# Performance work log

Hardware: AMD Instinct MI355X
Metric: run time of the kernel (lower is better)

The kernel has to match this reference:

```python
import jax, jax.numpy as jnp
import numpy as np

NEG_SLOPE = 0.2  # PyG GATConv default leaky_relu slope


def _add_self_loops(edge_index, num_nodes):
    loop = jnp.arange(num_nodes, dtype=edge_index.dtype)
    return jnp.concatenate([edge_index, jnp.stack([loop, loop])], axis=1)


def _gat_conv(x, edge_index, W, a_src, a_dst, b, heads, out_c):
    # x: [N, Fin]; W: [Fin, heads*out_c]; a_src/a_dst: [heads, out_c]; b: [heads*out_c]
    N = x.shape[0]
    h = (x @ W).reshape(N, heads, out_c)                       # [N,H,C]
    src, dst = edge_index[0], edge_index[1]
    alpha_src = jnp.einsum('nhc,hc->nh', h, a_src)             # [N,H]
    alpha_dst = jnp.einsum('nhc,hc->nh', h, a_dst)             # [N,H]
    e = jax.nn.leaky_relu(alpha_src[src] + alpha_dst[dst], NEG_SLOPE)  # [E,H]
    # segment softmax over edges grouped by destination node
    m = jax.ops.segment_max(e, dst, num_segments=N)
    m = jnp.where(jnp.isfinite(m), m, jnp.zeros_like(m))
    ex = jnp.exp(e - m[dst])
    denom = jax.ops.segment_sum(ex, dst, num_segments=N)
    alpha = ex / (denom[dst] + 1e-16)                          # [E,H]
    out = jax.ops.segment_sum(h[src] * alpha[:, :, None], dst, num_segments=N)
    return out.reshape(N, heads * out_c) + b


def setup_inputs() -> dict:
    key = jax.random.key(0)
    ks = jax.random.split(key, 16)
    N, E, FIN, HID, HEADS, OUT = 50000, 800000, 128, 32, 4, 64
    x = jax.random.normal(ks[0], (N, FIN), dtype=jnp.float32)
    edge_index = jax.random.randint(ks[1], (2, E), 0, N, dtype=jnp.int64)
    s = 0.1
    inp = {
        'x': x, 'edge_index': edge_index,
        'W0': jax.random.normal(ks[2], (FIN, HEADS * HID), jnp.float32) * s,
        'asrc0': jax.random.normal(ks[3], (HEADS, HID), jnp.float32) * s,
        'adst0': jax.random.normal(ks[4], (HEADS, HID), jnp.float32) * s,
        'b0': jnp.zeros((HEADS * HID,), jnp.float32),
        'W1': jax.random.normal(ks[5], (HEADS * HID, HEADS * HID), jnp.float32) * s,
        'asrc1': jax.random.normal(ks[6], (HEADS, HID), jnp.float32) * s,
        'adst1': jax.random.normal(ks[7], (HEADS, HID), jnp.float32) * s,
        'b1': jnp.zeros((HEADS * HID,), jnp.float32),
        'W2': jax.random.normal(ks[8], (HEADS * HID, OUT), jnp.float32) * s,
        'asrc2': jax.random.normal(ks[9], (1, OUT), jnp.float32) * s,
        'adst2': jax.random.normal(ks[10], (1, OUT), jnp.float32) * s,
        'b2': jnp.zeros((OUT,), jnp.float32),
    }
    return inp


def reference(x, edge_index, W0, asrc0, adst0, b0, W1, asrc1, adst1, b1, W2, asrc2, adst2, b2):
    # Dropout is identity in eval mode.
    N = x.shape[0]
    ei = _add_self_loops(edge_index, N)
    h = _gat_conv(x, ei, W0, asrc0, adst0, b0, heads=4, out_c=32)
    h = jax.nn.relu(h)
    h = _gat_conv(h, ei, W1, asrc1, adst1, b1, heads=4, out_c=32)
    h = jax.nn.relu(h)
    out = _gat_conv(h, ei, W2, asrc2, adst2, b2, heads=1, out_c=64)
    return out
```

## Files before the change

kernel.cpp:

```cpp
#include <hip/hip_runtime.h>


#define NEG_SLOPE 0.2f

typedef _Float16 f16;
typedef f16 f16x8 __attribute__((ext_vector_type(8)));
typedef f16 f16x4 __attribute__((ext_vector_type(4)));
typedef f16 f16x2 __attribute__((ext_vector_type(2)));
typedef float f32x4 __attribute__((ext_vector_type(4)));

#define BSH 6
#define DLOWM 63
#define KEYBITS 22

__device__ __forceinline__ float lrelu(float v) { return v > 0.f ? v : NEG_SLOPE * v; }


__global__ void fill_zero_kernel(int* __restrict__ p, int n) {
    int i = blockIdx.x * blockDim.x + threadIdx.x;
    if (i < n) p[i] = 0;
}

__global__ __launch_bounds__(256) void bucket_count_kernel(const int* __restrict__ dst, int E,
                                                           int NBK, int* __restrict__ bcount) {
    __shared__ int lh[1024];
#pragma unroll
    for (int j = 0; j < 4; ++j) lh[threadIdx.x + j * 256] = 0;
    __syncthreads();
    int stride = gridDim.x * 256 * 4;
    for (int i = (blockIdx.x * 256 + threadIdx.x) * 4; i < E; i += stride) {
        int4 d = *(const int4*)&dst[i];
        atomicAdd(&lh[d.x >> BSH], 1);
        atomicAdd(&lh[d.y >> BSH], 1);
        atomicAdd(&lh[d.z >> BSH], 1);
        atomicAdd(&lh[d.w >> BSH], 1);
    }
    __syncthreads();
#pragma unroll
    for (int j = 0; j < 4; ++j) {
        int idx = threadIdx.x + j * 256;
        if (idx < NBK) {
            int v = lh[idx];
            if (v > 0) atomicAdd(&bcount[idx], v);
        }
    }
}

__global__ __launch_bounds__(256) void bucket_scan_kernel(const int* __restrict__ bcount, int NBK,
                                                          int* __restrict__ bbase,
                                                          int* __restrict__ bcursor,
                                                          int* __restrict__ offsets, int N) {
    int t = threadIdx.x;
    int chunk = (NBK + 255) / 256;
    int b0 = t * chunk, b1 = b0 + chunk;
    if (b0 > NBK) b0 = NBK;
    if (b1 > NBK) b1 = NBK;
    int s = 0;
    for (int i = b0; i < b1; ++i) s += bcount[i];
    int v = s;
    int lane = t & 63, wid = t >> 6;
#pragma unroll
    for (int off = 1; off < 64; off <<= 1) {
        int u = __shfl_up(v, off);
        if (lane >= off) v += u;
    }
    __shared__ int ws[4];
    if (lane == 63) ws[wid] = v;
    __syncthreads();
    int add = 0;
    for (int w = 0; w < wid; ++w) add += ws[w];
    v += add;
    int prefix = v - s;
    for (int i = b0; i < b1; ++i) {
        bbase[i] = prefix;
        bcursor[i] = prefix;
        prefix += bcount[i];
    }
    if (t == 255) {
        bbase[NBK] = v;
        offsets[N] = v;
    }
}

#define SC_TILE 4096
__global__ __launch_bounds__(256) void bucket_scatter_kernel(const int* __restrict__ src,
                                                             const int* __restrict__ dst, int E,
                                                             int* __restrict__ bcursor,
                                                             unsigned int* __restrict__ staging) {
    __shared__ int lh[1024];
    __shared__ int lcur[1024];
    int tid = threadIdx.x;
#pragma unroll
    for (int j = 0; j < 4; ++j) lh[tid + j * 256] = 0;
    __syncthreads();
    int base = blockIdx.x * SC_TILE + tid * 16;
    int sv[16], dv[16];
    bool act = base < E;
    if (act) {
#pragma unroll
        for (int q = 0; q < 4; ++q) {
            *(int4*)&sv[q * 4] = *(const int4*)&src[base + q * 4];
            *(int4*)&dv[q * 4] = *(const int4*)&dst[base + q * 4];
        }
#pragma unroll
        for (int j = 0; j < 16; ++j) atomicAdd(&lh[dv[j] >> BSH], 1);
    }
    __syncthreads();
#pragma unroll
    for (int j = 0; j < 4; ++j) {
        int idx = tid + j * 256;
        int c = lh[idx];
        if (c > 0) lcur[idx] = atomicAdd(&bcursor[idx], c);
    }
    __syncthreads();
    if (act) {
#pragma unroll
        for (int j = 0; j < 16; ++j) {
            int b = dv[j] >> BSH;
            int pos = atomicAdd(&lcur[b], 1);
            staging[pos] = (unsigned int)sv[j] | ((unsigned int)(dv[j] & DLOWM) << 16);
        }
    }
}

#define SORT_CAP 2048
#define MIDX(f) ((f) + ((f) >> 4))
__global__ __launch_bounds__(256) void bucket_sort_kernel(const unsigned int* __restrict__ staging,
                                                          const int* __restrict__ bbase,
                                                          int* __restrict__ offsets,
                                                          int* __restrict__ ssrc, int N) {
    __shared__ unsigned int bufA[SORT_CAP];
    __shared__ unsigned int bufB[SORT_CAP];
    __shared__ int mat[4096 + 256];
    __shared__ int lh[64];
    __shared__ int wsum[4];
    int b = blockIdx.x;
    int tid = threadIdx.x;
    int s = bbase[b], e = bbase[b + 1];
    int cnt = e - s;
    bool fits = cnt <= SORT_CAP;

    if (tid < 64) lh[tid] = 0;
    __syncthreads();
    if (fits) {
        for (int i = tid; i < cnt; i += 256) {
            unsigned int r = staging[s + i];
            bufA[i] = r;
            atomicAdd(&lh[r >> 16], 1);
        }
    } else {
        for (int i = tid; i < cnt; i += 256) atomicAdd(&lh[staging[s + i] >> 16], 1);
    }
    __syncthreads();

    int exc0 = 0;
    if (tid < 64) {
        int own = lh[tid];
        int v = own;
#pragma unroll
        for (int off = 1; off < 64; off <<= 1) {
            int u = __shfl_up(v, off);
            if (tid >= off) v += u;
        }
        exc0 = v - own;
        int dstn = (b << BSH) + tid;
        if (dstn < N) offsets[dstn] = s + exc0;
    }
    __syncthreads();

    int lane = tid & 63, wid = tid >> 6;
    if (fits) {
        unsigned int* in = bufA;
        unsigned int* out = bufB;
        int L = (cnt + 255) >> 8;
        int i0 = tid * L;
        int i1 = i0 + L;
        if (i0 > cnt) i0 = cnt;
        if (i1 > cnt) i1 = cnt;
        for (int sh = 0; sh < KEYBITS; sh += 4) {
            int c16[16];
#pragma unroll
            for (int d = 0; d < 16; ++d) c16[d] = 0;
            for (int i = i0; i < i1; ++i) c16[(in[i] >> sh) & 15]++;
#pragma unroll
            for (int d = 0; d < 16; ++d) mat[MIDX(d * 256 + tid)] = c16[d];
            __syncthreads();
            int base = tid * 16;
            int loc[16];
            int ssum = 0;
#pragma unroll
            for (int j = 0; j < 16; ++j) {
                loc[j] = ssum;
                ssum += mat[MIDX(base + j)];
            }
            int vv = ssum;
#pragma unroll
            for (int off = 1; off < 64; off <<= 1) {
                int u = __shfl_up(vv, off);
                if (lane >= off) vv += u;
            }
            if (lane == 63) wsum[wid] = vv;
            __syncthreads();
            int add2 = 0;
            for (int w = 0; w < wid; ++w) add2 += wsum[w];
            int exc2 = vv + add2 - ssum;
#pragma unroll
            for (int j = 0; j < 16; ++j) mat[MIDX(base + j)] = exc2 + loc[j];
            __syncthreads();
#pragma unroll
            for (int d = 0; d < 16; ++d) c16[d] = mat[MIDX(d * 256 + tid)];
            for (int i = i0; i < i1; ++i) {
                unsigned int r = in[i];
                int d = (r >> sh) & 15;
                out[c16[d]++] = r;
            }
            __syncthreads();
            unsigned int* tmp = in;
            in = out;
            out = tmp;
        }
        for (int i = tid; i < cnt; i += 256) {
            unsigned int r = bufA[i];
            int dlow = (r >> 16) & DLOWM;
            unsigned int full = (r & 0xFFFFu) | ((unsigned int)((b << BSH) | dlow) << 16);
            ssrc[s + i] = (int)full;
        }
    } else {
        if (tid < 64) lh[tid] = exc0;
        __syncthreads();
        for (int i = tid; i < cnt; i += 256) {
            unsigned int rec = staging[s + i];
            int dlow = rec >> 16;
            int r = atomicAdd(&lh[dlow], 1);
            unsigned int full = (rec & 0xFFFFu) | ((unsigned int)((b << BSH) | dlow) << 16);
            ssrc[s + r] = (int)full;
        }
    }
}


__global__ void split_w_kernel(const float* __restrict__ W0, const float* __restrict__ W1,
                               const float* __restrict__ W2, f16* __restrict__ w0h,
                               f16* __restrict__ w0l, f16* __restrict__ w1h,
                               f16* __restrict__ w1l, f16* __restrict__ w2h,
                               f16* __restrict__ w2l) {
    int idx = blockIdx.x * 256 + threadIdx.x;
    if (idx < 16384) {
        int k = idx >> 7, c = idx & 127;
        float v = W0[k * 128 + c];
        f16 h = (f16)v;
        w0h[c * 128 + k] = h;
        w0l[c * 128 + k] = (f16)(v - (float)h);
    } else if (idx < 32768) {
        int t = idx - 16384;
        int k = t >> 7, c = t & 127;
        float v = W1[k * 128 + c];
        f16 h = (f16)v;
        w1h[c * 128 + k] = h;
        w1l[c * 128 + k] = (f16)(v - (float)h);
    } else if (idx < 40960) {
        int t = idx - 32768;
        int k = t >> 6, c = t & 63;
        float v = W2[k * 64 + c];
        f16 h = (f16)v;
        w2h[c * 128 + k] = h;
        w2l[c * 128 + k] = (f16)(v - (float)h);
    }
}

template <int FOUT, int H_, bool F32A>
__global__ __launch_bounds__(256) void gemm_mfma_kernel(
    const f16* __restrict__ Ah, const f16* __restrict__ Al, const float* __restrict__ Af,
    const f16* __restrict__ Bh, const f16* __restrict__ Bl, const float* __restrict__ a_src,
    const float* __restrict__ a_dst, f16* __restrict__ H16, float* __restrict__ asrc,
    float* __restrict__ adst, int N) {
    constexpr int CT = FOUT / 16;
    constexpr int TPH = CT / H_;
    __shared__ f16 lw[2][FOUT][72];
    int tid = threadIdx.x;
    int w = tid >> 6, lane = tid & 63;
    int quad = lane >> 4, m = lane & 15;
    int row0 = blockIdx.x * 64 + w * 16;
    int arow = row0 + m;
    if (arow >= N) arow = N - 1;
    const f16* aph = &Ah[(size_t)arow * 128 + quad * 8];
    const f16* apl = &Al[(size_t)arow * 128 + quad * 8];
    const float* apf = &Af[(size_t)arow * 128 + quad * 8];

    f32x4 acc[CT];
#pragma unroll
    for (int t = 0; t < CT; ++t) acc[t] = (f32x4){0.f, 0.f, 0.f, 0.f};

    for (int kh = 0; kh < 2; ++kh) {
        __syncthreads();
        for (int f = tid; f < FOUT * 8; f += 256) {
            int col = f >> 3, ch = f & 7;
            *(f16x8*)&lw[0][col][ch * 8] = *(const f16x8*)&Bh[(size_t)col * 128 + kh * 64 + ch * 8];
            *(f16x8*)&lw[1][col][ch * 8] = *(const f16x8*)&Bl[(size_t)col * 128 + kh * 64 + ch * 8];
        }
        __syncthreads();
#pragma unroll
        for (int kc = 0; kc < 2; ++kc) {
            f16x8 fah, fal;
            if (F32A) {
                const float* p = apf + kh * 64 + kc * 32;
                float4 v0 = *(const float4*)p;
                float4 v1 = *(const float4*)(p + 4);
                float vv[8] = {v0.x, v0.y, v0.z, v0.w, v1.x, v1.y, v1.z, v1.w};
#pragma unroll
                for (int j = 0; j < 8; ++j) {
                    f16 h = (f16)vv[j];
                    fah[j] = h;
                    fal[j] = (f16)(vv[j] - (float)h);
                }
            } else {
                fah = *(const f16x8*)&aph[kh * 64 + kc * 32];
                fal = *(const f16x8*)&apl[kh * 64 + kc * 32];
            }
#pragma unroll
            for (int t = 0; t < CT; ++t) {
                f16x8 fbh = *(const f16x8*)&lw[0][t * 16 + m][kc * 32 + quad * 8];
                f16x8 fbl = *(const f16x8*)&lw[1][t * 16 + m][kc * 32 + quad * 8];
                acc[t] = __builtin_amdgcn_mfma_f32_16x16x32_f16(fah, fbh, acc[t], 0, 0, 0);
                acc[t] = __builtin_amdgcn_mfma_f32_16x16x32_f16(fal, fbh, acc[t], 0, 0, 0);
                acc[t] = __builtin_amdgcn_mfma_f32_16x16x32_f16(fah, fbl, acc[t], 0, 0, 0);
            }
        }
    }

    float asf[CT], adf[CT];
#pragma unroll
    for (int t = 0; t < CT; ++t) {
        asf[t] = a_src[t * 16 + m];
        adf[t] = a_dst[t * 16 + m];
    }

#pragma unroll
    for (int r = 0; r < 4; ++r) {
        int row = row0 + quad * 4 + r;
        f16 hq[CT];
        float hr[CT];
#pragma unroll
        for (int t = 0; t < CT; ++t) {
            hq[t] = (f16)acc[t][r];
            hr[t] = (float)hq[t];
        }
        float pa[H_], pd[H_];
#pragma unroll
        for (int hh = 0; hh < H_; ++hh) {
            pa[hh] = 0.f;
            pd[hh] = 0.f;
#pragma unroll
            for (int tt = 0; tt < TPH; ++tt) {
                int t = hh * TPH + tt;
                pa[hh] += hr[t] * asf[t];
                pd[hh] += hr[t] * adf[t];
            }
        }
#pragma unroll
        for (int mask = 1; mask < 16; mask <<= 1) {
#pragma unroll
            for (int hh = 0; hh < H_; ++hh) {
                pa[hh] += __shfl_xor(pa[hh], mask);
                pd[hh] += __shfl_xor(pd[hh], mask);
            }
        }
        if (row < N) {
#pragma unroll
            for (int t = 0; t < CT; ++t) H16[(size_t)row * FOUT + t * 16 + m] = hq[t];
#pragma unroll
            for (int hh = 0; hh < H_; ++hh) {
                if (m == hh) {
                    asrc[row * H_ + hh] = pa[hh];
                    adst[row * H_ + hh] = pd[hh];
                }
            }
        }
    }
}

template <int H_, int C, bool RELU, bool SPLIT_OUT>
__global__ __launch_bounds__(256) void aggr_kernel(
    const f16* __restrict__ h16, const float* __restrict__ asrc,
    const float* __restrict__ adst, const float* __restrict__ bias,
    const int* __restrict__ offsets, const int* __restrict__ ssrc, float* __restrict__ outf,
    f16* __restrict__ outh, f16* __restrict__ outl, int N) {
    constexpr int FOUT = H_ * C;
    constexpr int LPG = FOUT / 8;
    constexpr int GROUPS = 64 / LPG;
    constexpr int UN = (GROUPS == 4) ? 4 : 2;
    int wid = threadIdx.x >> 6;
    int lane = threadIdx.x & 63;
    int n = blockIdx.x * 4 + wid;
    if (n >= N) return;
    int g = lane / LPG;
    int t = lane % LPG;
    int c0 = t * 8;
    int head = c0 / C;

    float adn = adst[n * H_ + head];
    float esf = lrelu(asrc[n * H_ + head] + adn);

    float D = 0.f;
    float S[8];
#pragma unroll
    for (int j = 0; j < 8; ++j) S[j] = 0.f;
    if (g == 0) {
        D = 1.f;
        f16x8 hv = *(const f16x8*)&h16[n * FOUT + c0];
#pragma unroll
        for (int j = 0; j < 8; ++j) S[j] = (float)hv[j];
    }

    int e1 = offsets[n + 1];
    int k = offsets[n] + g;

    for (; k < e1; k += UN * GROUPS) {
        int sarr[UN];
        bool valid[UN];
        float aval[UN];
        f16x8 hvv[UN];
#pragma unroll
        for (int u = 0; u < UN; ++u) {
            int kk = k + u * GROUPS;
            valid[u] = kk < e1;
            sarr[u] = ssrc[valid[u] ? kk : k] & 0xFFFF;
        }
#pragma unroll
        for (int u = 0; u < UN; ++u) {
            aval[u] = asrc[sarr[u] * H_ + head];
            hvv[u] = *(const f16x8*)&h16[sarr[u] * FOUT + c0];
        }
#pragma unroll
        for (int u = 0; u < UN; ++u) {
            float w = valid[u] ? __expf(lrelu(aval[u] + adn) - esf) : 0.f;
            D += w;
#pragma unroll
            for (int j = 0; j < 8; ++j) S[j] += w * (float)hvv[u][j];
        }
    }

#pragma unroll
    for (int mask = LPG; mask < 64; mask <<= 1) {
        D += __shfl_xor(D, mask);
#pragma unroll
        for (int j = 0; j < 8; ++j) S[j] += __shfl_xor(S[j], mask);
    }

    if (g == 0) {
        float inv = 1.f / (D + 1e-16f);
        float v[8];
#pragma unroll
        for (int j = 0; j < 8; ++j) {
            v[j] = S[j] * inv + bias[c0 + j];
            if (RELU) v[j] = fmaxf(v[j], 0.f);
        }
        if (SPLIT_OUT) {
            f16x8 hh, ll;
#pragma unroll
            for (int j = 0; j < 8; ++j) {
                f16 h = (f16)v[j];
                hh[j] = h;
                ll[j] = (f16)(v[j] - (float)h);
            }
            *(f16x8*)&outh[n * FOUT + c0] = hh;
            *(f16x8*)&outl[n * FOUT + c0] = ll;
        } else {
            *(float4*)&outf[n * FOUT + c0] = make_float4(v[0], v[1], v[2], v[3]);
            *(float4*)&outf[n * FOUT + c0 + 4] = make_float4(v[4], v[5], v[6], v[7]);
        }
    }
}

extern "C" void kernel_launch(void* const* d_in, const int* in_sizes, int n_in,
                              void* d_out, int out_size, void* d_ws, size_t ws_size,
                              hipStream_t stream) {
    const float* x = (const float*)d_in[0];
    const int* ei = (const int*)d_in[1];
    const float* W0 = (const float*)d_in[2];
    const float* as0 = (const float*)d_in[3];
    const float* ad0 = (const float*)d_in[4];
    const float* b0 = (const float*)d_in[5];
    const float* W1 = (const float*)d_in[6];
    const float* as1 = (const float*)d_in[7];
    const float* ad1 = (const float*)d_in[8];
    const float* b1 = (const float*)d_in[9];
    const float* W2 = (const float*)d_in[10];
    const float* as2 = (const float*)d_in[11];
    const float* ad2 = (const float*)d_in[12];
    const float* b2 = (const float*)d_in[13];

    const int N = in_sizes[0] / 128;
    const int E = in_sizes[1] / 2;
    const int NBK = (N + (1 << BSH) - 1) >> BSH;

    float* aS = (float*)d_ws;
    float* aD = aS + (size_t)N * 4;
    f16* h16 = (f16*)(aD + (size_t)N * 4);
    f16* xh = h16 + (size_t)N * 128;
    f16* xl = xh + (size_t)N * 128;
    f16* w0h = xl + (size_t)N * 128;
    f16* w0l = w0h + 16384;
    f16* w1h = w0l + 16384;
    f16* w1l = w1h + 16384;
    f16* w2h = w1l + 16384;
    f16* w2l = w2h + 8192;
    int* offsets = (int*)(w2l + 8192);
    int* ssrc = offsets + N + 1;
    unsigned int* staging = (unsigned int*)(ssrc + E);
    int* bcount = (int*)(staging + E);
    int* bbase = bcount + NBK;
    int* bcursor = bbase + NBK + 1;

    fill_zero_kernel<<<(NBK + 255) / 256, 256, 0, stream>>>(bcount, NBK);
    bucket_count_kernel<<<196, 256, 0, stream>>>(ei + E, E, NBK, bcount);
    bucket_scan_kernel<<<1, 256, 0, stream>>>(bcount, NBK, bbase, bcursor, offsets, N);
    bucket_scatter_kernel<<<(E + SC_TILE - 1) / SC_TILE, 256, 0, stream>>>(ei, ei + E, E, bcursor,
                                                                           staging);
    bucket_sort_kernel<<<NBK, 256, 0, stream>>>(staging, bbase, offsets, ssrc, N);

    split_w_kernel<<<160, 256, 0, stream>>>(W0, W1, W2, w0h, w0l, w1h, w1l, w2h, w2l);

    const int gGemm = (N + 63) / 64;
    const int gAggr = (N + 3) / 4;

    gemm_mfma_kernel<128, 4, true><<<gGemm, 256, 0, stream>>>(nullptr, nullptr, x, w0h, w0l, as0,
                                                              ad0, h16, aS, aD, N);
    aggr_kernel<4, 32, true, true><<<gAggr, 256, 0, stream>>>(h16, aS, aD, b0, offsets, ssrc,
                                                              nullptr, xh, xl, N);
    gemm_mfma_kernel<128, 4, false><<<gGemm, 256, 0, stream>>>(xh, xl, nullptr, w1h, w1l, as1,
                                                               ad1, h16, aS, aD, N);
    aggr_kernel<4, 32, true, true><<<gAggr, 256, 0, stream>>>(h16, aS, aD, b1, offsets, ssrc,
                                                              nullptr, xh, xl, N);
    gemm_mfma_kernel<64, 1, false><<<gGemm, 256, 0, stream>>>(xh, xl, nullptr, w2h, w2l, as2,
                                                              ad2, h16, aS, aD, N);
    aggr_kernel<1, 64, false, false><<<gAggr, 256, 0, stream>>>(h16, aS, aD, b2, offsets, ssrc,
                                                                (float*)d_out, nullptr, nullptr,
                                                                N);
}
```

Baseline: 293.5 us.

## Fuse bucket count and scan into layer-0 GEMM launch, zero counters in weight split

Measured after the change: 303.8 us. 3.5% more time.

```diff
diff --git a/kernel.cpp b/kernel.cpp
--- a/kernel.cpp
+++ b/kernel.cpp
@@ -12,75 +12,10 @@
 #define BSH 6
 #define DLOWM 63
 #define KEYBITS 22
+#define CNTB 196
 
 __device__ __forceinline__ float lrelu(float v) { return v > 0.f ? v : NEG_SLOPE * v; }
 
-
-__global__ void fill_zero_kernel(int* __restrict__ p, int n) {
-    int i = blockIdx.x * blockDim.x + threadIdx.x;
-    if (i < n) p[i] = 0;
-}
-
-__global__ __launch_bounds__(256) void bucket_count_kernel(const int* __restrict__ dst, int E,
-                                                           int NBK, int* __restrict__ bcount) {
-    __shared__ int lh[1024];
-#pragma unroll
-    for (int j = 0; j < 4; ++j) lh[threadIdx.x + j * 256] = 0;
-    __syncthreads();
-    int stride = gridDim.x * 256 * 4;
-    for (int i = (blockIdx.x * 256 + threadIdx.x) * 4; i < E; i += stride) {
-        int4 d = *(const int4*)&dst[i];
-        atomicAdd(&lh[d.x >> BSH], 1);
-        atomicAdd(&lh[d.y >> BSH], 1);
-        atomicAdd(&lh[d.z >> BSH], 1);
-        atomicAdd(&lh[d.w >> BSH], 1);
-    }
-    __syncthreads();
-#pragma unroll
-    for (int j = 0; j < 4; ++j) {
-        int idx = threadIdx.x + j * 256;
-        if (idx < NBK) {
-            int v = lh[idx];
-            if (v > 0) atomicAdd(&bcount[idx], v);
-        }
-    }
-}
-
-__global__ __launch_bounds__(256) void bucket_scan_kernel(const int* __restrict__ bcount, int NBK,
-                                                          int* __restrict__ bbase,
-                                                          int* __restrict__ bcursor,
-                                                          int* __restrict__ offsets, int N) {
-    int t = threadIdx.x;
-    int chunk = (NBK + 255) / 256;
-    int b0 = t * chunk, b1 = b0 + chunk;
-    if (b0 > NBK) b0 = NBK;
-    if (b1 > NBK) b1 = NBK;
-    int s = 0;
-    for (int i = b0; i < b1; ++i) s += bcount[i];
-    int v = s;
-    int lane = t & 63, wid = t >> 6;
-#pragma unroll
-    for (int off = 1; off < 64; off <<= 1) {
-        int u = __shfl_up(v, off);
-        if (lane >= off) v += u;
-    }
-    __shared__ int ws[4];
-    if (lane == 63) ws[wid] = v;
-    __syncthreads();
-    int add = 0;
-    for (int w = 0; w < wid; ++w) add += ws[w];
-    v += add;
-    int prefix = v - s;
-    for (int i = b0; i < b1; ++i) {
-        bbase[i] = prefix;
-        bcursor[i] = prefix;
-        prefix += bcount[i];
-    }
-    if (t == 255) {
-        bbase[NBK] = v;
-        offsets[N] = v;
-    }
-}
 
 #define SC_TILE 4096
 __global__ __launch_bounds__(256) void bucket_scatter_kernel(const int* __restrict__ src,
@@ -243,8 +178,11 @@
                                const float* __restrict__ W2, f16* __restrict__ w0h,
                                f16* __restrict__ w0l, f16* __restrict__ w1h,
                                f16* __restrict__ w1l, f16* __restrict__ w2h,
-                               f16* __restrict__ w2l) {
+                               f16* __restrict__ w2l, int* __restrict__ bcount, int NBK,
+                               int* __restrict__ done) {
     int idx = blockIdx.x * 256 + threadIdx.x;
+    if (idx < NBK) bcount[idx] = 0;
+    if (idx == 0) *done = 0;
     if (idx < 16384) {
         int k = idx >> 7, c = idx & 127;
         float v = W0[k * 128 + c];
@@ -268,12 +206,184 @@
     }
 }
 
-template <int FOUT, int H_, bool F32A>
+__global__ __launch_bounds__(256) void gemm0_csr_kernel(
+    const float* __restrict__ Af, const f16* __restrict__ Bh, const f16* __restrict__ Bl,
+    const float* __restrict__ a_src, const float* __restrict__ a_dst, f16* __restrict__ H16,
+    float* __restrict__ asrc, float* __restrict__ adst, int N, int gG,
+    const int* __restrict__ dstarr, int E, int NBK, int* __restrict__ bcount,
+    int* __restrict__ done, int* __restrict__ bbase, int* __restrict__ bcursor,
+    int* __restrict__ offsets) {
+    constexpr int FOUT = 128, H_ = 4, CT = 8, TPH = 2;
+    __shared__ __align__(16) char shraw[2 * FOUT * 72 * 2];
+    int tid = threadIdx.x;
+
+    if (blockIdx.x < gG) {
+        f16(*lw)[FOUT][72] = reinterpret_cast<f16(*)[FOUT][72]>(shraw);
+        int w = tid >> 6, lane = tid & 63;
+        int quad = lane >> 4, m = lane & 15;
+        int row0 = blockIdx.x * 64 + w * 16;
+        int arow = row0 + m;
+        if (arow >= N) arow = N - 1;
+        const float* apf = &Af[(size_t)arow * 128 + quad * 8];
+
+        f32x4 acc[CT];
+#pragma unroll
+        for (int t = 0; t < CT; ++t) acc[t] = (f32x4){0.f, 0.f, 0.f, 0.f};
+
+        for (int kh = 0; kh < 2; ++kh) {
+            __syncthreads();
+            for (int f = tid; f < FOUT * 8; f += 256) {
+                int col = f >> 3, ch = f & 7;
+                *(f16x8*)&lw[0][col][ch * 8] =
+                    *(const f16x8*)&Bh[(size_t)col * 128 + kh * 64 + ch * 8];
+                *(f16x8*)&lw[1][col][ch * 8] =
+                    *(const f16x8*)&Bl[(size_t)col * 128 + kh * 64 + ch * 8];
+            }
+            __syncthreads();
+#pragma unroll
+            for (int kc = 0; kc < 2; ++kc) {
+                f16x8 fah, fal;
+                const float* p = apf + kh * 64 + kc * 32;
+                float4 v0 = *(const float4*)p;
+                float4 v1 = *(const float4*)(p + 4);
+                float vv[8] = {v0.x, v0.y, v0.z, v0.w, v1.x, v1.y, v1.z, v1.w};
+#pragma unroll
+                for (int j = 0; j < 8; ++j) {
+                    f16 h = (f16)vv[j];
+                    fah[j] = h;
+                    fal[j] = (f16)(vv[j] - (float)h);
+                }
+#pragma unroll
+                for (int t = 0; t < CT; ++t) {
+                    f16x8 fbh = *(const f16x8*)&lw[0][t * 16 + m][kc * 32 + quad * 8];
+                    f16x8 fbl = *(const f16x8*)&lw[1][t * 16 + m][kc * 32 + quad * 8];
+                    acc[t] = __builtin_amdgcn_mfma_f32_16x16x32_f16(fah, fbh, acc[t], 0, 0, 0);
+                    acc[t] = __builtin_amdgcn_mfma_f32_16x16x32_f16(fal, fbh, acc[t], 0, 0, 0);
+                    acc[t] = __builtin_amdgcn_mfma_f32_16x16x32_f16(fah, fbl, acc[t], 0, 0, 0);
+                }
+            }
+        }
+
+        float asf[CT], adf[CT];
+#pragma unroll
+        for (int t = 0; t < CT; ++t) {
+            asf[t] = a_src[t * 16 + m];
+            adf[t] = a_dst[t * 16 + m];
+        }
+
+#pragma unroll
+        for (int r = 0; r < 4; ++r) {
+            int row = row0 + quad * 4 + r;
+            f16 hq[CT];
+            float hr[CT];
+#pragma unroll
+            for (int t = 0; t < CT; ++t) {
+                hq[t] = (f16)acc[t][r];
+                hr[t] = (float)hq[t];
+            }
+            float pa[H_], pd[H_];
+#pragma unroll
+            for (int hh = 0; hh < H_; ++hh) {
+                pa[hh] = 0.f;
+                pd[hh] = 0.f;
+#pragma unroll
+                for (int tt = 0; tt < TPH; ++tt) {
+                    int t = hh * TPH + tt;
+                    pa[hh] += hr[t] * asf[t];
+                    pd[hh] += hr[t] * adf[t];
+                }
+            }
+#pragma unroll
+            for (int mask = 1; mask < 16; mask <<= 1) {
+#pragma unroll
+                for (int hh = 0; hh < H_; ++hh) {
+                    pa[hh] += __shfl_xor(pa[hh], mask);
+                    pd[hh] += __shfl_xor(pd[hh], mask);
+                }
+            }
+            if (row < N) {
+#pragma unroll
+                for (int t = 0; t < CT; ++t) H16[(size_t)row * FOUT + t * 16 + m] = hq[t];
+#pragma unroll
+                for (int hh = 0; hh < H_; ++hh) {
+                    if (m == hh) {
+                        asrc[row * H_ + hh] = pa[hh];
+                        adst[row * H_ + hh] = pd[hh];
+                    }
+                }
+            }
+        }
+    } else {
+        int* lh = (int*)shraw;
+        int* flag = (int*)(shraw + 8192);
+#pragma unroll
+        for (int j = 0; j < 4; ++j) lh[tid + j * 256] = 0;
+        __syncthreads();
+        int cb = blockIdx.x - gG;
+        int stride = CNTB * 256 * 4;
+        for (int i = (cb * 256 + tid) * 4; i < E; i += stride) {
+            int4 d = *(const int4*)&dstarr[i];
+            atomicAdd(&lh[d.x >> BSH], 1);
+            atomicAdd(&lh[d.y >> BSH], 1);
+            atomicAdd(&lh[d.z >> BSH], 1);
+            atomicAdd(&lh[d.w >> BSH], 1);
+        }
+        __syncthreads();
+#pragma unroll
+        for (int j = 0; j < 4; ++j) {
+            int idx = tid + j * 256;
+            if (idx < NBK) {
+                int v = lh[idx];
+                if (v > 0) atomicAdd(&bcount[idx], v);
+            }
+        }
+        __threadfence();
+        __syncthreads();
+        if (tid == 0) *flag = (atomicAdd(done, 1) == CNTB - 1) ? 1 : 0;
+        __syncthreads();
+        if (*flag) {
+            int chunk = (NBK + 255) / 256;
+            int b0 = tid * chunk, b1 = b0 + chunk;
+            if (b0 > NBK) b0 = NBK;
+            if (b1 > NBK) b1 = NBK;
+            int cvals[4];
+            int s = 0;
+            for (int i = b0; i < b1; ++i) {
+                cvals[i - b0] = atomicAdd(&bcount[i], 0);
+                s += cvals[i - b0];
+            }
+            int v = s;
+            int lane = tid & 63, wid = tid >> 6;
+#pragma unroll
+            for (int off = 1; off < 64; off <<= 1) {
+                int u = __shfl_up(v, off);
+                if (lane >= off) v += u;
+            }
+            int* ws4 = (int*)(shraw + 8320);
+            if (lane == 63) ws4[wid] = v;
+            __syncthreads();
+            int add = 0;
+            for (int w = 0; w < wid; ++w) add += ws4[w];
+            v += add;
+            int prefix = v - s;
+            for (int i = b0; i < b1; ++i) {
+                bbase[i] = prefix;
+                bcursor[i] = prefix;
+                prefix += cvals[i - b0];
+            }
+            if (tid == 255) {
+                bbase[NBK] = v;
+                offsets[N] = v;
+            }
+        }
+    }
+}
+
+template <int FOUT, int H_>
 __global__ __launch_bounds__(256) void gemm_mfma_kernel(
-    const f16* __restrict__ Ah, const f16* __restrict__ Al, const float* __restrict__ Af,
-    const f16* __restrict__ Bh, const f16* __restrict__ Bl, const float* __restrict__ a_src,
-    const float* __restrict__ a_dst, f16* __restrict__ H16, float* __restrict__ asrc,
-    float* __restrict__ adst, int N) {
+    const f16* __restrict__ Ah, const f16* __restrict__ Al, const f16* __restrict__ Bh,
+    const f16* __restrict__ Bl, const float* __restrict__ a_src, const float* __restrict__ a_dst,
+    f16* __restrict__ H16, float* __restrict__ asrc, float* __restrict__ adst, int N) {
     constexpr int CT = FOUT / 16;
     constexpr int TPH = CT / H_;
     __shared__ f16 lw[2][FOUT][72];
@@ -285,7 +395,6 @@
     if (arow >= N) arow = N - 1;
     const f16* aph = &Ah[(size_t)arow * 128 + quad * 8];
     const f16* apl = &Al[(size_t)arow * 128 + quad * 8];
-    const float* apf = &Af[(size_t)arow * 128 + quad * 8];
 
     f32x4 acc[CT];
 #pragma unroll
@@ -301,22 +410,8 @@
         __syncthreads();
 #pragma unroll
         for (int kc = 0; kc < 2; ++kc) {
-            f16x8 fah, fal;
-            if (F32A) {
-                const float* p = apf + kh * 64 + kc * 32;
-                float4 v0 = *(const float4*)p;
-                float4 v1 = *(const float4*)(p + 4);
-                float vv[8] = {v0.x, v0.y, v0.z, v0.w, v1.x, v1.y, v1.z, v1.w};
-#pragma unroll
-                for (int j = 0; j < 8; ++j) {
-                    f16 h = (f16)vv[j];
-                    fah[j] = h;
-                    fal[j] = (f16)(vv[j] - (float)h);
-                }
-            } else {
-                fah = *(const f16x8*)&aph[kh * 64 + kc * 32];
-                fal = *(const f16x8*)&apl[kh * 64 + kc * 32];
-            }
+            f16x8 fah = *(const f16x8*)&aph[kh * 64 + kc * 32];
+            f16x8 fal = *(const f16x8*)&apl[kh * 64 + kc * 32];
 #pragma unroll
             for (int t = 0; t < CT; ++t) {
                 f16x8 fbh = *(const f16x8*)&lw[0][t * 16 + m][kc * 32 + quad * 8];
@@ -511,29 +606,26 @@
     int* bcount = (int*)(staging + E);
     int* bbase = bcount + NBK;
     int* bcursor = bbase + NBK + 1;
-
-    fill_zero_kernel<<<(NBK + 255) / 256, 256, 0, stream>>>(bcount, NBK);
-    bucket_count_kernel<<<196, 256, 0, stream>>>(ei + E, E, NBK, bcount);
-    bucket_scan_kernel<<<1, 256, 0, stream>>>(bcount, NBK, bbase, bcursor, offsets, N);
+    int* done = bcursor + NBK;
+
+    const int gGemm = (N + 63) / 64;
+    const int gAggr = (N + 3) / 4;
+
+    split_w_kernel<<<160, 256, 0, stream>>>(W0, W1, W2, w0h, w0l, w1h, w1l, w2h, w2l,
+                                            bcount, NBK, done);
+    gemm0_csr_kernel<<<gGemm + CNTB, 256, 0, stream>>>(x, w0h, w0l, as0, ad0, h16, aS, aD, N,
+                                                       gGemm, ei + E, E, NBK, bcount, done,
+                                                       bbase, bcursor, offsets);
     bucket_scatter_kernel<<<(E + SC_TILE - 1) / SC_TILE, 256, 0, stream>>>(ei, ei + E, E, bcursor,
                                                                            staging);
     bucket_sort_kernel<<<NBK, 256, 0, stream>>>(staging, bbase, offsets, ssrc, N);
 
-    split_w_kernel<<<160, 256, 0, stream>>>(W0, W1, W2, w0h, w0l, w1h, w1l, w2h, w2l);
-
-    const int gGemm = (N + 63) / 64;
-    const int gAggr = (N + 3) / 4;
-
-    gemm_mfma_kernel<128, 4, true><<<gGemm, 256, 0, stream>>>(nullptr, nullptr, x, w0h, w0l, as0,
-                                                              ad0, h16, aS, aD, N);
     aggr_kernel<4, 32, true, true><<<gAggr, 256, 0, stream>>>(h16, aS, aD, b0, offsets, ssrc,
                                                               nullptr, xh, xl, N);
-    gemm_mfma_kernel<128, 4, false><<<gGemm, 256, 0, stream>>>(xh, xl, nullptr, w1h, w1l, as1,
-                                                               ad1, h16, aS, aD, N);
+    gemm_mfma_kernel<128, 4><<<gGemm, 256, 0, stream>>>(xh, xl, w1h, w1l, as1, ad1, h16, aS, aD, N);
     aggr_kernel<4, 32, true, true><<<gAggr, 256, 0, stream>>>(h16, aS, aD, b1, offsets, ssrc,
                                                               nullptr, xh, xl, N);
-    gemm_mfma_kernel<64, 1, false><<<gGemm, 256, 0, stream>>>(xh, xl, nullptr, w2h, w2l, as2,
-                                                              ad2, h16, aS, aD, N);
+    gemm_mfma_kernel<64, 1><<<gGemm, 256, 0, stream>>>(xh, xl, w2h, w2l, as2, ad2, h16, aS, aD, N);
     aggr_kernel<1, 64, false, false><<<gAggr, 256, 0, stream>>>(h16, aS, aD, b2, offsets, ssrc,
                                                                 (float*)d_out, nullptr, nullptr,
                                                                 N);
```
